# Kernel tuning notes

Measured on AMD Instinct MI355X. Metric: run time of the kernel, lower is better.

## Reference

```python
import jax, jax.numpy as jnp
import numpy as np

MARGIN = 0.2
N = 512
D = 128
N_CLASSES = 64


def setup_inputs() -> dict:
    key = jax.random.key(0)
    k1, k2 = jax.random.split(key)
    z = jax.random.normal(k1, (N, D), dtype=jnp.float32)
    labels = jax.random.randint(k2, (N,), 0, N_CLASSES)
    return {"z": z, "labels": labels}


def _pdist(x, y):
    sq = (jnp.sum(x * x, axis=1)[:, None]
          + jnp.sum(y * y, axis=1)[None, :]
          - 2.0 * (x @ y.T))
    sq = jnp.maximum(sq, 0.0)
    pos = sq > 0
    # safe sqrt (diagonal is exactly 0; avoid inf gradient there)
    return jnp.sqrt(jnp.where(pos, sq, 1.0)) * pos


def reference(z, labels):
    n = labels.shape[0]
    d = _pdist(z, z)                                  # [N, N]
    same = labels[None, :] == labels[:, None]         # [N, N]
    diff = ~same
    same = same & ~jnp.eye(n, dtype=bool)             # fill_diagonal_(False)
    # valid triplet mask [anchor, pos, neg]
    mask = same[:, :, None] & diff[:, None, :]        # [N, N, N] bool
    # d(a,p) - d(a,n) + margin over all (a,p,n)
    losses = d[:, :, None] - d[:, None, :] + MARGIN   # [N, N, N]
    n_eg = jnp.sum((losses > 0) & mask)
    n_triplets = jnp.sum(mask).astype(losses.dtype)
    loss = jnp.sum(jnp.where(mask, jax.nn.relu(losses), 0.0)) / n_triplets
    return loss, n_eg
```

## Files before the change

kernel.cpp:

```cpp
#include <hip/hip_runtime.h>

#define NPTS 512
#define DIM 128
#define MARGIN 0.2f
#define ATILE 2
#define NBLK (NPTS / ATILE)
#define TROWS 128
#define NTILE (NPTS / TROWS)

__global__ __launch_bounds__(512) void triplet_partial_kernel(
    const float* __restrict__ z, const int* __restrict__ labels,
    float* __restrict__ psum, unsigned* __restrict__ pcnt,
    unsigned* __restrict__ pntrip)
{
    __shared__ float4 stage[TROWS * 32];
    __shared__ float part[4][TROWS][ATILE];
    __shared__ float drow[ATILE][NPTS];
    __shared__ __align__(16) float pdm[ATILE][NPTS];
    __shared__ int wcnt[ATILE][8];
    __shared__ float red_f[8];
    __shared__ unsigned red_c[8];

    const int t = threadIdx.x;
    const int a0 = blockIdx.x * ATILE;
    const int wid = t >> 6, lane = t & 63;
    const int q = t >> 7;
    const int r = t & (TROWS - 1);

    const float4* zg = reinterpret_cast<const float4*>(z);

    float4 za[ATILE][8];
    #pragma unroll
    for (int i = 0; i < ATILE; ++i)
        #pragma unroll
        for (int kk = 0; kk < 8; ++kk)
            za[i][kk] = zg[(size_t)(a0 + i) * 32 + q * 8 + kk];

    for (int T = 0; T < NTILE; ++T) {
        #pragma unroll
        for (int p = 0; p < 8; ++p) {
            int f = p * 512 + t;
            int row = f >> 5, chunk = f & 31;
            stage[row * 32 + (chunk ^ (row & 7))] =
                zg[(size_t)(T * TROWS + row) * 32 + chunk];
        }
        __syncthreads();

        float acc0 = 0.f, acc1 = 0.f;
        const int rx = r & 7;
        #pragma unroll
        for (int kk = 0; kk < 8; ++kk) {
            float4 v = stage[r * 32 + ((q * 8 + kk) ^ rx)];
            float4 w0 = za[0][kk], w1 = za[1][kk];
            float d0 = w0.x - v.x, d1 = w0.y - v.y, d2 = w0.z - v.z, d3 = w0.w - v.w;
            acc0 += d0 * d0 + d1 * d1 + d2 * d2 + d3 * d3;
            float e0 = w1.x - v.x, e1 = w1.y - v.y, e2 = w1.z - v.z, e3 = w1.w - v.w;
            acc1 += e0 * e0 + e1 * e1 + e2 * e2 + e3 * e3;
        }
        part[q][r][0] = acc0;
        part[q][r][1] = acc1;
        __syncthreads();

        if (t < TROWS) {
            float s0 = part[0][t][0] + part[1][t][0] + part[2][t][0] + part[3][t][0];
            float s1 = part[0][t][1] + part[1][t][1] + part[2][t][1] + part[3][t][1];
            drow[0][T * TROWS + t] = sqrtf(s0);
            drow[1][T * TROWS + t] = sqrtf(s1);
        }
    }
    __syncthreads();

    const int lt = labels[t];
    int la[ATILE];
    #pragma unroll
    for (int i = 0; i < ATILE; ++i) la[i] = labels[a0 + i];

    bool pred[ATILE];
    unsigned long long m[ATILE];
    #pragma unroll
    for (int i = 0; i < ATILE; ++i) {
        pred[i] = (lt == la[i]) && (t != a0 + i);
        m[i] = __ballot(pred[i]);
        if (lane == 0) wcnt[i][wid] = (int)__popcll(m[i]);
    }
    __syncthreads();

    unsigned np[ATILE], npad[ATILE];
    #pragma unroll
    for (int i = 0; i < ATILE; ++i) {
        unsigned base = 0, n = 0;
        #pragma unroll
        for (int w = 0; w < 8; ++w) {
            unsigned c = (unsigned)wcnt[i][w];
            if (w < wid) base += c;
            n += c;
        }
        np[i] = n;
        npad[i] = (n + 3u) & ~3u;
        if (pred[i])
            pdm[i][base + __popcll(m[i] & ((1ull << lane) - 1ull))] = drow[i][t] + MARGIN;
        if ((unsigned)t >= n && (unsigned)t < npad[i])
            pdm[i][t] = -1e30f;
    }
    __syncthreads();

    float sum = 0.f;
    unsigned cnt = 0;
    #pragma unroll
    for (int i = 0; i < ATILE; ++i) {
        if (lt != la[i]) {
            const float si = drow[i][t];
            const float4* p4 = reinterpret_cast<const float4*>(pdm[i]);
            const int n4 = (int)(npad[i] >> 2);
            for (int p = 0; p < n4; ++p) {
                float4 qv = p4[p];
                float v0 = qv.x - si, v1 = qv.y - si, v2 = qv.z - si, v3 = qv.w - si;
                if (v0 > 0.f) { sum += v0; ++cnt; }
                if (v1 > 0.f) { sum += v1; ++cnt; }
                if (v2 > 0.f) { sum += v2; ++cnt; }
                if (v3 > 0.f) { sum += v3; ++cnt; }
            }
        }
    }

    #pragma unroll
    for (int off = 32; off > 0; off >>= 1) {
        sum += __shfl_down(sum, off, 64);
        cnt += __shfl_down(cnt, off, 64);
    }
    if (lane == 0) { red_f[wid] = sum; red_c[wid] = cnt; }
    __syncthreads();
    if (t == 0) {
        float S = 0.f;
        unsigned C = 0;
        #pragma unroll
        for (int w = 0; w < 8; ++w) { S += red_f[w]; C += red_c[w]; }
        unsigned NT = 0;
        #pragma unroll
        for (int i = 0; i < ATILE; ++i) NT += np[i] * (unsigned)(NPTS - 1 - np[i]);
        psum[blockIdx.x] = S;
        pcnt[blockIdx.x] = C;
        pntrip[blockIdx.x] = NT;
    }
}

__global__ __launch_bounds__(256) void triplet_final_kernel(
    const float* __restrict__ psum, const unsigned* __restrict__ pcnt,
    const unsigned* __restrict__ pntrip, float* __restrict__ out)
{
    __shared__ float rf[4];
    __shared__ unsigned rc[4], rn[4];

    const int t = threadIdx.x;
    float s = psum[t];
    unsigned c = pcnt[t];
    unsigned nt = pntrip[t];

    #pragma unroll
    for (int off = 32; off > 0; off >>= 1) {
        s  += __shfl_down(s,  off, 64);
        c  += __shfl_down(c,  off, 64);
        nt += __shfl_down(nt, off, 64);
    }
    const int wid = t >> 6, lane = t & 63;
    if (lane == 0) { rf[wid] = s; rc[wid] = c; rn[wid] = nt; }
    __syncthreads();
    if (t == 0) {
        double S = 0.0;
        unsigned C = 0, NT = 0;
        #pragma unroll
        for (int w = 0; w < 4; ++w) { S += (double)rf[w]; C += rc[w]; NT += rn[w]; }
        out[0] = (float)(S / (double)NT);
        out[1] = (float)C;
    }
}

extern "C" void kernel_launch(void* const* d_in, const int* in_sizes, int n_in,
                              void* d_out, int out_size, void* d_ws, size_t ws_size,
                              hipStream_t stream) {
    const float* z = (const float*)d_in[0];
    const int* labels = (const int*)d_in[1];
    float* out = (float*)d_out;

    float* psum = (float*)d_ws;
    unsigned* pcnt = (unsigned*)((char*)d_ws + NBLK * sizeof(float));
    unsigned* pntrip = pcnt + NBLK;

    triplet_partial_kernel<<<NBLK, 512, 0, stream>>>(z, labels, psum, pcnt, pntrip);
    triplet_final_kernel<<<1, NBLK, 0, stream>>>(psum, pcnt, pntrip, out);
}
```

Measured before the change: 15.43 us.

## Fuse final reduction via last-block atomic counter and double-buffer tile loads

Merges the two-kernel reduction into one kernel: each block publishes partials and bumps an atomic counter, and the last block does the final reduction. Tile staging now uses direct global-to-LDS loads into a double buffer, prefetching the next tile during compute. The per-row sqrt reduction is spread over 256 threads. A memset is added to reset the counter, which adds a launch/operation, and LDS usage roughly doubles for staging.

```diff
diff --git a/kernel.cpp b/kernel.cpp
--- a/kernel.cpp
+++ b/kernel.cpp
@@ -8,26 +8,42 @@
 #define TROWS 128
 #define NTILE (NPTS / TROWS)
 
-__global__ __launch_bounds__(512) void triplet_partial_kernel(
+__device__ __forceinline__ void gload_lds16(const float4* src, float4* dst) {
+    __builtin_amdgcn_global_load_lds(
+        (const __attribute__((address_space(1))) void*)src,
+        (__attribute__((address_space(3))) void*)dst, 16, 0, 0);
+}
+
+__global__ __launch_bounds__(512) void triplet_fused_kernel(
     const float* __restrict__ z, const int* __restrict__ labels,
     float* __restrict__ psum, unsigned* __restrict__ pcnt,
-    unsigned* __restrict__ pntrip)
+    unsigned* __restrict__ pntrip, unsigned* __restrict__ counter,
+    float* __restrict__ out)
 {
-    __shared__ float4 stage[TROWS * 32];
-    __shared__ float part[4][TROWS][ATILE];
+    __shared__ float4 stage[2][TROWS * 32];
+    __shared__ float part[4][TROWS][2];
     __shared__ float drow[ATILE][NPTS];
     __shared__ __align__(16) float pdm[ATILE][NPTS];
     __shared__ int wcnt[ATILE][8];
     __shared__ float red_f[8];
-    __shared__ unsigned red_c[8];
+    __shared__ unsigned red_c[8], red_n[8];
+    __shared__ unsigned lastFlag;
 
     const int t = threadIdx.x;
-    const int a0 = blockIdx.x * ATILE;
+    const int b = blockIdx.x;
+    const int a0 = b * ATILE;
     const int wid = t >> 6, lane = t & 63;
     const int q = t >> 7;
     const int r = t & (TROWS - 1);
+    const int lane5 = lane & 31;
+    const int lh = lane >> 5;
 
     const float4* zg = reinterpret_cast<const float4*>(z);
+
+    const int lt = labels[t];
+    int la[ATILE];
+    #pragma unroll
+    for (int i = 0; i < ATILE; ++i) la[i] = labels[a0 + i];
 
     float4 za[ATILE][8];
     #pragma unroll
@@ -36,21 +52,29 @@
         for (int kk = 0; kk < 8; ++kk)
             za[i][kk] = zg[(size_t)(a0 + i) * 32 + q * 8 + kk];
 
+    #pragma unroll
+    for (int p = 0; p < 8; ++p) {
+        int row = (wid << 4) + (p << 1) + lh;
+        int srcu = row * 32 + (lane5 ^ (row & 7));
+        gload_lds16(zg + srcu, &stage[0][(wid << 9) + (p << 6)]);
+    }
+    __syncthreads();
+
+    const int rx = r & 7;
     for (int T = 0; T < NTILE; ++T) {
-        #pragma unroll
-        for (int p = 0; p < 8; ++p) {
-            int f = p * 512 + t;
-            int row = f >> 5, chunk = f & 31;
-            stage[row * 32 + (chunk ^ (row & 7))] =
-                zg[(size_t)(T * TROWS + row) * 32 + chunk];
-        }
-        __syncthreads();
-
+        const int cur = T & 1;
+        if (T + 1 < NTILE) {
+            #pragma unroll
+            for (int p = 0; p < 8; ++p) {
+                int row = (wid << 4) + (p << 1) + lh;
+                int srcu = ((T + 1) * TROWS + row) * 32 + (lane5 ^ (row & 7));
+                gload_lds16(zg + srcu, &stage[cur ^ 1][(wid << 9) + (p << 6)]);
+            }
+        }
         float acc0 = 0.f, acc1 = 0.f;
-        const int rx = r & 7;
         #pragma unroll
         for (int kk = 0; kk < 8; ++kk) {
-            float4 v = stage[r * 32 + ((q * 8 + kk) ^ rx)];
+            float4 v = stage[cur][r * 32 + ((q * 8 + kk) ^ rx)];
             float4 w0 = za[0][kk], w1 = za[1][kk];
             float d0 = w0.x - v.x, d1 = w0.y - v.y, d2 = w0.z - v.z, d3 = w0.w - v.w;
             acc0 += d0 * d0 + d1 * d1 + d2 * d2 + d3 * d3;
@@ -60,20 +84,14 @@
         part[q][r][0] = acc0;
         part[q][r][1] = acc1;
         __syncthreads();
-
-        if (t < TROWS) {
-            float s0 = part[0][t][0] + part[1][t][0] + part[2][t][0] + part[3][t][0];
-            float s1 = part[0][t][1] + part[1][t][1] + part[2][t][1] + part[3][t][1];
-            drow[0][T * TROWS + t] = sqrtf(s0);
-            drow[1][T * TROWS + t] = sqrtf(s1);
-        }
-    }
-    __syncthreads();
-
-    const int lt = labels[t];
-    int la[ATILE];
-    #pragma unroll
-    for (int i = 0; i < ATILE; ++i) la[i] = labels[a0 + i];
+        if (t < 2 * TROWS) {
+            int rr = t & (TROWS - 1), ii = t >> 7;
+            float s = part[0][rr][ii] + part[1][rr][ii]
+                    + part[2][rr][ii] + part[3][rr][ii];
+            drow[ii][T * TROWS + rr] = sqrtf(s);
+        }
+        __syncthreads();
+    }
 
     bool pred[ATILE];
     unsigned long long m[ATILE];
@@ -130,6 +148,7 @@
     }
     if (lane == 0) { red_f[wid] = sum; red_c[wid] = cnt; }
     __syncthreads();
+
     if (t == 0) {
         float S = 0.f;
         unsigned C = 0;
@@ -138,40 +157,41 @@
         unsigned NT = 0;
         #pragma unroll
         for (int i = 0; i < ATILE; ++i) NT += np[i] * (unsigned)(NPTS - 1 - np[i]);
-        psum[blockIdx.x] = S;
-        pcnt[blockIdx.x] = C;
-        pntrip[blockIdx.x] = NT;
-    }
-}
-
-__global__ __launch_bounds__(256) void triplet_final_kernel(
-    const float* __restrict__ psum, const unsigned* __restrict__ pcnt,
-    const unsigned* __restrict__ pntrip, float* __restrict__ out)
-{
-    __shared__ float rf[4];
-    __shared__ unsigned rc[4], rn[4];
-
-    const int t = threadIdx.x;
-    float s = psum[t];
-    unsigned c = pcnt[t];
-    unsigned nt = pntrip[t];
-
-    #pragma unroll
-    for (int off = 32; off > 0; off >>= 1) {
-        s  += __shfl_down(s,  off, 64);
-        c  += __shfl_down(c,  off, 64);
-        nt += __shfl_down(nt, off, 64);
-    }
-    const int wid = t >> 6, lane = t & 63;
-    if (lane == 0) { rf[wid] = s; rc[wid] = c; rn[wid] = nt; }
-    __syncthreads();
-    if (t == 0) {
-        double S = 0.0;
-        unsigned C = 0, NT = 0;
-        #pragma unroll
-        for (int w = 0; w < 4; ++w) { S += (double)rf[w]; C += rc[w]; NT += rn[w]; }
-        out[0] = (float)(S / (double)NT);
-        out[1] = (float)C;
+        __hip_atomic_store(&psum[b], S, __ATOMIC_RELAXED, __HIP_MEMORY_SCOPE_AGENT);
+        __hip_atomic_store(&pcnt[b], C, __ATOMIC_RELAXED, __HIP_MEMORY_SCOPE_AGENT);
+        __hip_atomic_store(&pntrip[b], NT, __ATOMIC_RELAXED, __HIP_MEMORY_SCOPE_AGENT);
+        unsigned old = __hip_atomic_fetch_add(counter, 1u, __ATOMIC_ACQ_REL,
+                                              __HIP_MEMORY_SCOPE_AGENT);
+        lastFlag = (old == NBLK - 1) ? 1u : 0u;
+    }
+    __syncthreads();
+
+    if (lastFlag) {
+        float s = 0.f;
+        unsigned c = 0, nt = 0;
+        if (t < NBLK) {
+            s  = __hip_atomic_load(&psum[t],   __ATOMIC_RELAXED, __HIP_MEMORY_SCOPE_AGENT);
+            c  = __hip_atomic_load(&pcnt[t],   __ATOMIC_RELAXED, __HIP_MEMORY_SCOPE_AGENT);
+            nt = __hip_atomic_load(&pntrip[t], __ATOMIC_RELAXED, __HIP_MEMORY_SCOPE_AGENT);
+        }
+        #pragma unroll
+        for (int off = 32; off > 0; off >>= 1) {
+            s  += __shfl_down(s,  off, 64);
+            c  += __shfl_down(c,  off, 64);
+            nt += __shfl_down(nt, off, 64);
+        }
+        if (lane == 0) { red_f[wid] = s; red_c[wid] = c; red_n[wid] = nt; }
+        __syncthreads();
+        if (t == 0) {
+            double S = 0.0;
+            unsigned C = 0, NT = 0;
+            #pragma unroll
+            for (int w = 0; w < 4; ++w) {
+                S += (double)red_f[w]; C += red_c[w]; NT += red_n[w];
+            }
+            out[0] = (float)(S / (double)NT);
+            out[1] = (float)C;
+        }
     }
 }
 
@@ -182,10 +202,12 @@
     const int* labels = (const int*)d_in[1];
     float* out = (float*)d_out;
 
-    float* psum = (float*)d_ws;
-    unsigned* pcnt = (unsigned*)((char*)d_ws + NBLK * sizeof(float));
-    unsigned* pntrip = pcnt + NBLK;
-
-    triplet_partial_kernel<<<NBLK, 512, 0, stream>>>(z, labels, psum, pcnt, pntrip);
-    triplet_final_kernel<<<1, NBLK, 0, stream>>>(psum, pcnt, pntrip, out);
+    unsigned* counter = (unsigned*)d_ws;
+    float* psum = (float*)((char*)d_ws + 16);
+    unsigned* pcnt = (unsigned*)((char*)d_ws + 16 + NBLK * 4);
+    unsigned* pntrip = (unsigned*)((char*)d_ws + 16 + NBLK * 8);
+
+    hipMemsetAsync(counter, 0, sizeof(unsigned), stream);
+    triplet_fused_kernel<<<NBLK, 512, 0, stream>>>(z, labels, psum, pcnt, pntrip,
+                                                   counter, out);
 }
```

Measured after the change: 23.32 us. 51.2% more time.

## Double-buffer z tiles with direct global-to-LDS loads and shuffle-reduce distances

Applied to the files above, without the earlier changes.

Staging of z row tiles into shared memory now uses global_load_lds with a two-buffer ring, so the next tile loads while the current one is consumed. Thread mapping is changed so the four partial sums for a row sit in adjacent lanes, and they are combined with xor shuffles instead of a shared-memory partial array and a second pass. This removes one barrier per tile plus the LDS round trip, and label loads are hoisted earlier. The risk is whether the async LDS loads are correctly ordered by the single barrier per iteration, since there is no explicit vmcnt wait.

```diff
diff --git a/kernel.cpp b/kernel.cpp
--- a/kernel.cpp
+++ b/kernel.cpp
@@ -7,14 +7,20 @@
 #define NBLK (NPTS / ATILE)
 #define TROWS 128
 #define NTILE (NPTS / TROWS)
-
-__global__ __launch_bounds__(512) void triplet_partial_kernel(
+#define NTHR 512
+
+__device__ __forceinline__ void gload_lds16(const float4* src, float4* dst) {
+    __builtin_amdgcn_global_load_lds(
+        (const __attribute__((address_space(1))) void*)src,
+        (__attribute__((address_space(3))) void*)dst, 16, 0, 0);
+}
+
+__global__ __launch_bounds__(NTHR) void triplet_partial_kernel(
     const float* __restrict__ z, const int* __restrict__ labels,
     float* __restrict__ psum, unsigned* __restrict__ pcnt,
     unsigned* __restrict__ pntrip)
 {
-    __shared__ float4 stage[TROWS * 32];
-    __shared__ float part[4][TROWS][ATILE];
+    __shared__ float4 stage[2][TROWS * 32];
     __shared__ float drow[ATILE][NPTS];
     __shared__ __align__(16) float pdm[ATILE][NPTS];
     __shared__ int wcnt[ATILE][8];
@@ -22,12 +28,20 @@
     __shared__ unsigned red_c[8];
 
     const int t = threadIdx.x;
-    const int a0 = blockIdx.x * ATILE;
+    const int b = blockIdx.x;
+    const int a0 = b * ATILE;
     const int wid = t >> 6, lane = t & 63;
-    const int q = t >> 7;
-    const int r = t & (TROWS - 1);
+    const int r = t >> 2;
+    const int q = t & 3;
+    const int rx = r & 7;
+    const int lane5 = lane & 31, lh = lane >> 5;
 
     const float4* zg = reinterpret_cast<const float4*>(z);
+
+    const int lt = labels[t];
+    int la[ATILE];
+    #pragma unroll
+    for (int i = 0; i < ATILE; ++i) la[i] = labels[a0 + i];
 
     float4 za[ATILE][8];
     #pragma unroll
@@ -36,44 +50,44 @@
         for (int kk = 0; kk < 8; ++kk)
             za[i][kk] = zg[(size_t)(a0 + i) * 32 + q * 8 + kk];
 
+    #pragma unroll
+    for (int p = 0; p < 8; ++p) {
+        int row = (wid << 4) + (p << 1) + lh;
+        int srcu = row * 32 + (lane5 ^ (row & 7));
+        gload_lds16(zg + srcu, &stage[0][(wid << 9) + (p << 6)]);
+    }
+    __syncthreads();
+
     for (int T = 0; T < NTILE; ++T) {
-        #pragma unroll
-        for (int p = 0; p < 8; ++p) {
-            int f = p * 512 + t;
-            int row = f >> 5, chunk = f & 31;
-            stage[row * 32 + (chunk ^ (row & 7))] =
-                zg[(size_t)(T * TROWS + row) * 32 + chunk];
-        }
-        __syncthreads();
-
+        const int cur = T & 1;
+        if (T + 1 < NTILE) {
+            #pragma unroll
+            for (int p = 0; p < 8; ++p) {
+                int row = (wid << 4) + (p << 1) + lh;
+                int srcu = ((T + 1) * TROWS + row) * 32 + (lane5 ^ (row & 7));
+                gload_lds16(zg + srcu, &stage[cur ^ 1][(wid << 9) + (p << 6)]);
+            }
+        }
         float acc0 = 0.f, acc1 = 0.f;
-        const int rx = r & 7;
         #pragma unroll
         for (int kk = 0; kk < 8; ++kk) {
-            float4 v = stage[r * 32 + ((q * 8 + kk) ^ rx)];
+            float4 v = stage[cur][r * 32 + ((q * 8 + kk) ^ rx)];
             float4 w0 = za[0][kk], w1 = za[1][kk];
             float d0 = w0.x - v.x, d1 = w0.y - v.y, d2 = w0.z - v.z, d3 = w0.w - v.w;
             acc0 += d0 * d0 + d1 * d1 + d2 * d2 + d3 * d3;
             float e0 = w1.x - v.x, e1 = w1.y - v.y, e2 = w1.z - v.z, e3 = w1.w - v.w;
             acc1 += e0 * e0 + e1 * e1 + e2 * e2 + e3 * e3;
         }
-        part[q][r][0] = acc0;
-        part[q][r][1] = acc1;
+        acc0 += __shfl_xor(acc0, 1, 64);
+        acc0 += __shfl_xor(acc0, 2, 64);
+        acc1 += __shfl_xor(acc1, 1, 64);
+        acc1 += __shfl_xor(acc1, 2, 64);
+        if (q == 0) {
+            drow[0][T * TROWS + r] = sqrtf(acc0);
+            drow[1][T * TROWS + r] = sqrtf(acc1);
+        }
         __syncthreads();
-
-        if (t < TROWS) {
-            float s0 = part[0][t][0] + part[1][t][0] + part[2][t][0] + part[3][t][0];
-            float s1 = part[0][t][1] + part[1][t][1] + part[2][t][1] + part[3][t][1];
-            drow[0][T * TROWS + t] = sqrtf(s0);
-            drow[1][T * TROWS + t] = sqrtf(s1);
-        }
-    }
-    __syncthreads();
-
-    const int lt = labels[t];
-    int la[ATILE];
-    #pragma unroll
-    for (int i = 0; i < ATILE; ++i) la[i] = labels[a0 + i];
+    }
 
     bool pred[ATILE];
     unsigned long long m[ATILE];
@@ -138,9 +152,9 @@
         unsigned NT = 0;
         #pragma unroll
         for (int i = 0; i < ATILE; ++i) NT += np[i] * (unsigned)(NPTS - 1 - np[i]);
-        psum[blockIdx.x] = S;
-        pcnt[blockIdx.x] = C;
-        pntrip[blockIdx.x] = NT;
+        psum[b] = S;
+        pcnt[b] = C;
+        pntrip[b] = NT;
     }
 }
 
@@ -186,6 +200,6 @@
     unsigned* pcnt = (unsigned*)((char*)d_ws + NBLK * sizeof(float));
     unsigned* pntrip = pcnt + NBLK;
 
-    triplet_partial_kernel<<<NBLK, 512, 0, stream>>>(z, labels, psum, pcnt, pntrip);
+    triplet_partial_kernel<<<NBLK, NTHR, 0, stream>>>(z, labels, psum, pcnt, pntrip);
     triplet_final_kernel<<<1, NBLK, 0, stream>>>(psum, pcnt, pntrip, out);
 }
```

New measurement: 18.06 us. 1.17x slower.
